# Performance work log

Measured on AMD Instinct MI355X. Metric: run time of the kernel, lower is better.

Reference implementation:

```python
import jax, jax.numpy as jnp
import numpy as np
from functools import partial

B, C, H, W = 16, 512, 38, 50
IMG_H, IMG_W = 608, 800
STRIDE = 16
IMG_SCALE = 1.0
MIN_SIZE = 16.0 * IMG_SCALE
PRE_NMS_TOP_N = 6000
POST_NMS_TOP_N = 300
NMS_THRESH = 0.7


def generate_anchor_base(base_size=16.0, ratios=(0.5, 1.0, 2.0), scales=(8.0, 16.0, 32.0)):
    # chainercv-style base anchors centered at (base/2, base/2), y1x1y2x2
    py = px = base_size / 2.0
    out = []
    for r in ratios:
        for s in scales:
            h = base_size * s * np.sqrt(r)
            w = base_size * s * np.sqrt(1.0 / r)
            out.append([py - h / 2, px - w / 2, py + h / 2, px + w / 2])
    return jnp.asarray(np.array(out, dtype=np.float32))  # [9, 4]


def all_anchors(anchor_base, stride, h, w):
    sy = jnp.arange(h, dtype=jnp.float32) * stride
    sx = jnp.arange(w, dtype=jnp.float32) * stride
    yy, xx = jnp.meshgrid(sy, sx, indexing='ij')
    shifts = jnp.stack([yy, xx, yy, xx], axis=-1).reshape(-1, 1, 4)  # [H*W,1,4]
    return (shifts + anchor_base[None]).reshape(-1, 4)  # [H*W*9, 4]


def conv2d(x, w, b, pad):
    y = jax.lax.conv_general_dilated(
        x, w, window_strides=(1, 1), padding=[(pad, pad), (pad, pad)],
        dimension_numbers=('NCHW', 'OIHW', 'NCHW'))
    return y + b[None, :, None, None]


def decode_boxes(anchors, loc):
    # anchors [N,4] y1x1y2x2, loc [B,N,4] (dy,dx,dh,dw)
    ah = anchors[:, 2] - anchors[:, 0]
    aw = anchors[:, 3] - anchors[:, 1]
    acy = anchors[:, 0] + 0.5 * ah
    acx = anchors[:, 1] + 0.5 * aw
    cy = loc[..., 0] * ah + acy
    cx = loc[..., 1] * aw + acx
    h = jnp.exp(loc[..., 2]) * ah
    w = jnp.exp(loc[..., 3]) * aw
    return jnp.stack([cy - 0.5 * h, cx - 0.5 * w, cy + 0.5 * h, cx + 0.5 * w], axis=-1)


def nms_fixed(boxes, scores, iou_thresh, max_out):
    # boxes [N,4], scores [N] (-inf = invalid); greedy NMS, fixed max_out steps
    areas = jnp.clip(boxes[:, 2] - boxes[:, 0], 0) * jnp.clip(boxes[:, 3] - boxes[:, 1], 0)

    def step(valid, _):
        s = jnp.where(valid, scores, -jnp.inf)
        i = jnp.argmax(s)
        ok = jnp.isfinite(s[i])
        box = boxes[i]
        yy1 = jnp.maximum(box[0], boxes[:, 0])
        xx1 = jnp.maximum(box[1], boxes[:, 1])
        yy2 = jnp.minimum(box[2], boxes[:, 2])
        xx2 = jnp.minimum(box[3], boxes[:, 3])
        inter = jnp.clip(yy2 - yy1, 0) * jnp.clip(xx2 - xx1, 0)
        iou = inter / (areas + areas[i] - inter + 1e-9)
        valid = valid & (iou <= iou_thresh)
        valid = valid.at[i].set(False)
        return valid, (i, ok)

    valid0 = jnp.isfinite(scores)
    _, (idx, ok) = jax.lax.scan(step, valid0, None, length=max_out)
    return idx, ok


def proposal_single(boxes, scores):
    # boxes [N,4], scores [N] for one image
    # clip to image
    boxes = jnp.stack([
        jnp.clip(boxes[:, 0], 0.0, IMG_H), jnp.clip(boxes[:, 1], 0.0, IMG_W),
        jnp.clip(boxes[:, 2], 0.0, IMG_H), jnp.clip(boxes[:, 3], 0.0, IMG_W)], axis=-1)
    hs = boxes[:, 2] - boxes[:, 0]
    ws = boxes[:, 3] - boxes[:, 1]
    keep = (hs >= MIN_SIZE) & (ws >= MIN_SIZE)
    scores = jnp.where(keep, scores, -jnp.inf)
    top_s, top_i = jax.lax.top_k(scores, PRE_NMS_TOP_N)
    top_b = boxes[top_i]
    idx, ok = nms_fixed(top_b, top_s, NMS_THRESH, POST_NMS_TOP_N)
    okf = ok.astype(boxes.dtype)
    rois = top_b[idx] * okf[:, None]
    rsc = jnp.where(ok, top_s[idx], 0.0)
    return jnp.concatenate([rois, rsc[:, None]], axis=-1)  # [POST, 5]


def setup_inputs() -> dict:
    key = jax.random.key(0)
    ks = jax.random.split(key, 7)
    return {
        'x': jax.random.normal(ks[0], (B, C, H, W), jnp.float32),
        'share_w': jax.random.normal(ks[1], (512, 512, 3, 3), jnp.float32) * 0.02,
        'share_b': jnp.zeros((512,), jnp.float32),
        'cls_w': jax.random.normal(ks[2], (18, 512, 1, 1), jnp.float32) * 0.02,
        'cls_b': jnp.zeros((18,), jnp.float32),
        'reg_w': jax.random.normal(ks[3], (36, 512, 1, 1), jnp.float32) * 0.02,
        'reg_b': jnp.zeros((36,), jnp.float32),
    }


def reference(x, share_w, share_b, cls_w, cls_b, reg_w, reg_b):
    anchors = all_anchors(generate_anchor_base(), STRIDE, H, W)  # [H*W*9, 4]
    shared = jax.nn.relu(conv2d(x, share_w, share_b, 1))
    cls = conv2d(shared, cls_w, cls_b, 0)           # [B,18,H,W]
    # note: original _reshape is a no-op (view result discarded), so softmax is over all 18 channels
    cls = jax.nn.softmax(cls, axis=1)
    reg = conv2d(shared, reg_w, reg_b, 0)           # [B,36,H,W]
    # foreground scores: [B,18,H,W] -> [B,H,W,9,2] -> fg channel
    scores = cls.transpose(0, 2, 3, 1).reshape(B, H * W * 9, 2)[..., 1]
    loc = reg.transpose(0, 2, 3, 1).reshape(B, H * W * 9, 4)
    boxes = decode_boxes(anchors, loc)              # [B,N,4]
    rois = jax.vmap(proposal_single)(boxes, scores)  # [B,POST,5]
    return rois
```

## Files before the change

kernel.cpp:

```cpp
#include <hip/hip_runtime.h>
#include <math.h>

#define NB 16
#define NC 512
#define NH 38
#define NW 50
#define NHW 1900
#define NPOS 30400
#define NANCH 17100
#define PRE_N 6000
#define POST_N 300
#define KTOT 4608
#define NIT 576
#define IMGH 608.0f
#define IMGW 800.0f

__global__ __launch_bounds__(256, 4)
void conv_f64_v7(const float* __restrict__ x, const float* __restrict__ w,
                 const float* __restrict__ bias, float* __restrict__ out)
{
    const int b    = blockIdx.z;
    const int co0  = blockIdx.y * 128;
    const int pos0 = blockIdx.x * 64;

    __shared__ __align__(16) double Ad[2][8][130];
    __shared__ __align__(16) double Bd[2][8][64];

    const int tid = threadIdx.x;
    const int ty  = tid >> 4;
    const int tx  = tid & 15;

    double acc[8][4];
#pragma unroll
    for (int m = 0; m < 8; ++m)
#pragma unroll
        for (int n = 0; n < 4; ++n) acc[m][n] = 0.0;

    const float* xb = x + (size_t)b * NC * NHW;

    const int coiA = tid >> 1;
    const int k4A  = (tid & 1) * 4;
    const float* wptr = w + (size_t)(co0 + coiA) * KTOT + k4A;

    const int kkB  = tid >> 5;
    const int piB  = tid & 31;
    const int pB1  = pos0 + piB;
    const int pB2  = pos0 + piB + 32;
    const int py1  = pB1 / NW, px1 = pB1 - (pB1 / NW) * NW;
    const int py2  = pB2 / NW, px2 = pB2 - (pB2 / NW) * NW;
    const bool ok1 = pB1 < NHW;
    const bool ok2 = pB2 < NHW;

    int ci = 0;
    int ky = kkB / 3;
    int kx = kkB - 3 * (kkB / 3);
    const float* xci = xb;

    float4 wa = *reinterpret_cast<const float4*>(wptr);
    float bs0, bs1;
    {
        const int yy1 = py1 + ky - 1, xx1 = px1 + kx - 1;
        const int yy2 = py2 + ky - 1, xx2 = px2 + kx - 1;
        bs0 = (ok1 && (unsigned)yy1 < (unsigned)NH && (unsigned)xx1 < (unsigned)NW)
                  ? xci[yy1 * NW + xx1] : 0.f;
        bs1 = (ok2 && (unsigned)yy2 < (unsigned)NH && (unsigned)xx2 < (unsigned)NW)
                  ? xci[yy2 * NW + xx2] : 0.f;
    }
    {
        const bool wrap = (ky == 0) && (kx == 0);
        if (wrap) { ky = 2; kx = 2; }
        else {
            --kx;
            if (kx < 0) { kx = 2; --ky; }
            ++ci; xci += NHW;
        }
    }
    Ad[0][k4A + 0][coiA] = (double)wa.x;
    Ad[0][k4A + 1][coiA] = (double)wa.y;
    Ad[0][k4A + 2][coiA] = (double)wa.z;
    Ad[0][k4A + 3][coiA] = (double)wa.w;
    Bd[0][kkB][piB]      = (double)bs0;
    Bd[0][kkB][piB + 32] = (double)bs1;
    __syncthreads();

    int cur = 0;
    for (int it = 0; it < NIT; ++it) {
        const bool more = (it + 1) < NIT;
        if (more) {
            wptr += 8;
            wa = *reinterpret_cast<const float4*>(wptr);
            const int yy1 = py1 + ky - 1, xx1 = px1 + kx - 1;
            const int yy2 = py2 + ky - 1, xx2 = px2 + kx - 1;
            bs0 = (ok1 && (unsigned)yy1 < (unsigned)NH && (unsigned)xx1 < (unsigned)NW)
                      ? xci[yy1 * NW + xx1] : 0.f;
            bs1 = (ok2 && (unsigned)yy2 < (unsigned)NH && (unsigned)xx2 < (unsigned)NW)
                      ? xci[yy2 * NW + xx2] : 0.f;
            const bool wrap = (ky == 0) && (kx == 0);
            if (wrap) { ky = 2; kx = 2; }
            else {
                --kx;
                if (kx < 0) { kx = 2; --ky; }
                ++ci; xci += NHW;
            }
        }

#pragma unroll
        for (int kk = 0; kk < 8; ++kk) {
            double av[8], bv[4];
#pragma unroll
            for (int m = 0; m < 8; ++m) av[m] = Ad[cur][kk][ty * 8 + m];
#pragma unroll
            for (int n = 0; n < 4; ++n) bv[n] = Bd[cur][kk][n * 16 + tx];
#pragma unroll
            for (int m = 0; m < 8; ++m)
#pragma unroll
                for (int n = 0; n < 4; ++n) acc[m][n] += av[m] * bv[n];
        }

        if (more) {
            const int nb = cur ^ 1;
            Ad[nb][k4A + 0][coiA] = (double)wa.x;
            Ad[nb][k4A + 1][coiA] = (double)wa.y;
            Ad[nb][k4A + 2][coiA] = (double)wa.z;
            Ad[nb][k4A + 3][coiA] = (double)wa.w;
            Bd[nb][kkB][piB]      = (double)bs0;
            Bd[nb][kkB][piB + 32] = (double)bs1;
            __syncthreads();
        }
        cur ^= 1;
    }

#pragma unroll
    for (int m = 0; m < 8; ++m) {
        const int co = co0 + ty * 8 + m;
        const double bi = (double)bias[co];
        float* orow = out + ((size_t)b * NC + co) * NHW;
#pragma unroll
        for (int n = 0; n < 4; ++n) {
            const int pos = pos0 + n * 16 + tx;
            if (pos < NHW) {
                const double d = acc[m][n] + bi;
                orow[pos] = (float)(d > 0.0 ? d : 0.0);
            }
        }
    }
}

__global__ __launch_bounds__(256)
void head_f64(const float* __restrict__ act,
              const float* __restrict__ cls_w, const float* __restrict__ cls_b,
              const float* __restrict__ reg_w, const float* __restrict__ reg_b,
              float* __restrict__ boxes, float* __restrict__ scores)
{
    const int p = blockIdx.x * 256 + threadIdx.x;
    if (p >= NPOS) return;
    const int b  = p / NHW;
    const int hw = p - b * NHW;

    const float* av = act + (size_t)b * NC * NHW + hw;

    double acc[54];
#pragma unroll
    for (int o = 0; o < 54; ++o) acc[o] = 0.0;

    for (int c = 0; c < NC; ++c) {
        const double v = (double)av[(size_t)c * NHW];
#pragma unroll
        for (int o = 0; o < 18; ++o) acc[o]      += v * (double)cls_w[o * NC + c];
#pragma unroll
        for (int o = 0; o < 36; ++o) acc[18 + o] += v * (double)reg_w[o * NC + c];
    }

    float lg[18];
#pragma unroll
    for (int o = 0; o < 18; ++o) lg[o] = (float)(acc[o] + (double)cls_b[o]);
    float loc[36];
#pragma unroll
    for (int o = 0; o < 36; ++o) loc[o] = (float)(acc[18 + o] + (double)reg_b[o]);

    double mx = -1e300;
#pragma unroll
    for (int o = 0; o < 18; ++o) mx = fmax(mx, (double)lg[o]);
    double sum = 0.0;
#pragma unroll
    for (int o = 0; o < 18; ++o) sum += exp((double)lg[o] - mx);
    const double inv = 1.0 / sum;

    const int hy = hw / NW;
    const int hx = hw - hy * NW;
    const float shy = (float)(hy * 16);
    const float shx = (float)(hx * 16);

    const double rats[3] = {0.5, 1.0, 2.0};
    const double scls[3] = {8.0, 16.0, 32.0};

#pragma unroll
    for (int a = 0; a < 9; ++a) {
        const int ir = a / 3, is = a - ir * 3;
        const double hh = 16.0 * scls[is] * sqrt(rats[ir]);
        const double wd = 16.0 * scls[is] * sqrt(1.0 / rats[ir]);
        const float ay1 = (float)(8.0 - hh * 0.5) + shy;
        const float ax1 = (float)(8.0 - wd * 0.5) + shx;
        const float ay2 = (float)(8.0 + hh * 0.5) + shy;
        const float ax2 = (float)(8.0 + wd * 0.5) + shx;
        const float ahf = ay2 - ay1;
        const float awf = ax2 - ax1;
        const float acy = ay1 + 0.5f * ahf;
        const float acx = ax1 + 0.5f * awf;

        const double ah = (double)ahf, aw = (double)awf;
        const double dy = (double)loc[4 * a + 0];
        const double dx = (double)loc[4 * a + 1];
        const double dh = (double)loc[4 * a + 2];
        const double dw = (double)loc[4 * a + 3];
        const double cy = dy * ah + (double)acy;
        const double cx = dx * aw + (double)acx;
        const double bh = exp(dh) * ah;
        const double bw = exp(dw) * aw;
        float y1 = (float)(cy - 0.5 * bh);
        float x1 = (float)(cx - 0.5 * bw);
        float y2 = (float)(cy + 0.5 * bh);
        float x2 = (float)(cx + 0.5 * bw);
        y1 = fminf(fmaxf(y1, 0.f), IMGH);
        y2 = fminf(fmaxf(y2, 0.f), IMGH);
        x1 = fminf(fmaxf(x1, 0.f), IMGW);
        x2 = fminf(fmaxf(x2, 0.f), IMGW);
        const bool keep = ((y2 - y1) >= 16.0f) && ((x2 - x1) >= 16.0f);

        float sc = (float)(exp((double)lg[2 * a + 1] - mx) * inv);
        if (!keep) sc = -INFINITY;

        const int n = hw * 9 + a;
        float4 bx; bx.x = y1; bx.y = x1; bx.z = y2; bx.w = x2;
        *reinterpret_cast<float4*>(&boxes[((size_t)b * NANCH + n) * 4]) = bx;
        scores[(size_t)b * NANCH + n] = sc;
    }
}

__global__ __launch_bounds__(256)
void rank2(const float* __restrict__ scores, const float* __restrict__ boxes,
           float* __restrict__ sortedS, float* __restrict__ sortedB)
{
    const int b = blockIdx.y;
    const int i = blockIdx.x * 256 + threadIdx.x;
    if (i >= NANCH) return;
    const float si = scores[(size_t)b * NANCH + i];
    const float* sb = scores + (size_t)b * NANCH;
    int rank = 0;
    for (int j = 0; j < NANCH; ++j) {
        const float sj = sb[j];
        rank += (sj > si) || (sj == si && j < i);
    }
    if (rank < PRE_N) {
        sortedS[(size_t)b * PRE_N + rank] = si;
        const float4 bx = *reinterpret_cast<const float4*>(&boxes[((size_t)b * NANCH + i) * 4]);
        *reinterpret_cast<float4*>(&sortedB[((size_t)b * PRE_N + rank) * 4]) = bx;
    }
}

__global__ __launch_bounds__(64)
void nms3(const float* __restrict__ sortedS, const float* __restrict__ sortedB,
          float* __restrict__ out)
{
    const int b    = blockIdx.x;
    const int lane = threadIdx.x;

    __shared__ float ky1[POST_N], kx1[POST_N], ky2[POST_N], kx2[POST_N];
    __shared__ float kar[POST_N], ksc[POST_N];
    __shared__ float cs[256];
    __shared__ float cb[256][4];

    const float* SS = sortedS + (size_t)b * PRE_N;
    const float* BB = sortedB + (size_t)b * PRE_N * 4;

    int nk = 0;
    bool done = false;
    for (int c0 = 0; c0 < PRE_N && !done; c0 += 256) {
        __syncthreads();
        for (int i = lane; i < 256; i += 64) {
            const int gi = c0 + i;
            if (gi < PRE_N) {
                cs[i] = SS[gi];
                const float4 bx = *reinterpret_cast<const float4*>(&BB[(size_t)gi * 4]);
                cb[i][0] = bx.x; cb[i][1] = bx.y; cb[i][2] = bx.z; cb[i][3] = bx.w;
            } else {
                cs[i] = -INFINITY;
                cb[i][0] = 0.f; cb[i][1] = 0.f; cb[i][2] = 0.f; cb[i][3] = 0.f;
            }
        }
        __syncthreads();

        for (int ic = 0; ic < 256; ++ic) {
            const float sc = cs[ic];
            if (sc == -INFINITY) { done = true; break; }
            const float y1 = cb[ic][0], x1 = cb[ic][1];
            const float y2 = cb[ic][2], x2 = cb[ic][3];
            const float areaC = fmaxf(y2 - y1, 0.f) * fmaxf(x2 - x1, 0.f);
            bool sup = false;
            for (int t = lane; t < nk; t += 64) {
                const float yy1 = fmaxf(y1, ky1[t]);
                const float xx1 = fmaxf(x1, kx1[t]);
                const float yy2 = fminf(y2, ky2[t]);
                const float xx2 = fminf(x2, kx2[t]);
                const float inter = fmaxf(yy2 - yy1, 0.f) * fmaxf(xx2 - xx1, 0.f);
                const float iou = inter / (areaC + kar[t] - inter + 1e-9f);
                if (iou > 0.7f) sup = true;
            }
            if (__ballot(sup) == 0ull) {
                if (lane == 0) {
                    ky1[nk] = y1; kx1[nk] = x1; ky2[nk] = y2; kx2[nk] = x2;
                    kar[nk] = areaC; ksc[nk] = sc;
                }
                __syncthreads();
                ++nk;
                if (nk == POST_N) { done = true; break; }
            }
        }
    }

    __syncthreads();
    for (int k2 = lane; k2 < POST_N; k2 += 64) {
        float o0 = 0.f, o1 = 0.f, o2 = 0.f, o3 = 0.f, o4 = 0.f;
        if (k2 < nk) {
            o0 = ky1[k2]; o1 = kx1[k2]; o2 = ky2[k2]; o3 = kx2[k2]; o4 = ksc[k2];
        }
        float* orow = out + ((size_t)b * POST_N + k2) * 5;
        orow[0] = o0; orow[1] = o1; orow[2] = o2; orow[3] = o3; orow[4] = o4;
    }
}

static const float* pick_input(void* const* d_in, const int* in_sizes, int n_in,
                               int want, int fallback)
{
    for (int i = 0; i < n_in; ++i)
        if (in_sizes[i] == want) return (const float*)d_in[i];
    return (const float*)d_in[fallback];
}

extern "C" void kernel_launch(void* const* d_in, const int* in_sizes, int n_in,
                              void* d_out, int out_size, void* d_ws, size_t ws_size,
                              hipStream_t stream)
{
    const float* x       = pick_input(d_in, in_sizes, n_in, 15564800, 0);
    const float* share_w = pick_input(d_in, in_sizes, n_in, 2359296, 1);
    const float* share_b = pick_input(d_in, in_sizes, n_in, 512, 2);
    const float* cls_w   = pick_input(d_in, in_sizes, n_in, 9216, 3);
    const float* cls_b   = pick_input(d_in, in_sizes, n_in, 18, 4);
    const float* reg_w   = pick_input(d_in, in_sizes, n_in, 18432, 5);
    const float* reg_b   = pick_input(d_in, in_sizes, n_in, 36, 6);
    float* out = (float*)d_out;

    float* W = (float*)d_ws;
    float* act     = W;
    float* boxes   = W + 15564800;
    float* scores  = W + 16659200;
    float* sortedB = W + 16932800;
    float* sortedS = W + 17316800;

    conv_f64_v7<<<dim3(30, 4, NB), 256, 0, stream>>>(x, share_w, share_b, act);

    head_f64<<<dim3(119), 256, 0, stream>>>(act, cls_w, cls_b, reg_w, reg_b,
                                            boxes, scores);

    rank2<<<dim3(67, 16), 256, 0, stream>>>(scores, boxes, sortedS, sortedB);

    nms3<<<dim3(16), 64, 0, stream>>>(sortedS, sortedB, out);
}
```

Baseline: 4.999 ms.

## Split 1x1 head convolution across output-channel groups into separate kernel

The 1x1 cls/reg head, which ran as 119 blocks each holding 54 double accumulators per thread, is split into a head_part kernel over a 119x6 grid that computes 9 output channels per thread and writes logits to a workspace buffer. A new decode_k kernel then reads those logits to do the softmax and box decoding. This is meant to raise parallelism and cut register pressure on an undersubscribed GPU. In exchange it adds an extra launch, a workspace round-trip for the logits, and reads the activations six times instead of once.

```diff
diff --git a/kernel.cpp b/kernel.cpp
--- a/kernel.cpp
+++ b/kernel.cpp
@@ -147,9 +147,46 @@
 }
 
 __global__ __launch_bounds__(256)
-void head_f64(const float* __restrict__ act,
-              const float* __restrict__ cls_w, const float* __restrict__ cls_b,
-              const float* __restrict__ reg_w, const float* __restrict__ reg_b,
+void head_part(const float* __restrict__ act,
+               const float* __restrict__ cls_w, const float* __restrict__ cls_b,
+               const float* __restrict__ reg_w, const float* __restrict__ reg_b,
+               float* __restrict__ hl)
+{
+    const int p = blockIdx.x * 256 + threadIdx.x;
+    if (p >= NPOS) return;
+    const int g  = blockIdx.y;
+    const int b  = p / NHW;
+    const int hw = p - b * NHW;
+
+    const float* av = act + (size_t)b * NC * NHW + hw;
+
+    const float* wrow[9];
+    double bia[9];
+#pragma unroll
+    for (int j = 0; j < 9; ++j) {
+        const int o = g * 9 + j;
+        if (o < 18) { wrow[j] = cls_w + (size_t)o * NC;        bia[j] = (double)cls_b[o]; }
+        else        { wrow[j] = reg_w + (size_t)(o - 18) * NC; bia[j] = (double)reg_b[o - 18]; }
+    }
+
+    double acc[9];
+#pragma unroll
+    for (int j = 0; j < 9; ++j) acc[j] = 0.0;
+
+    for (int c = 0; c < NC; ++c) {
+        const double v = (double)av[(size_t)c * NHW];
+#pragma unroll
+        for (int j = 0; j < 9; ++j) acc[j] += v * (double)wrow[j][c];
+    }
+
+    float* hb = hl + (size_t)b * 54 * NHW + hw;
+#pragma unroll
+    for (int j = 0; j < 9; ++j)
+        hb[(size_t)(g * 9 + j) * NHW] = (float)(acc[j] + bia[j]);
+}
+
+__global__ __launch_bounds__(256)
+void decode_k(const float* __restrict__ hl,
               float* __restrict__ boxes, float* __restrict__ scores)
 {
     const int p = blockIdx.x * 256 + threadIdx.x;
@@ -157,26 +194,14 @@
     const int b  = p / NHW;
     const int hw = p - b * NHW;
 
-    const float* av = act + (size_t)b * NC * NHW + hw;
-
-    double acc[54];
-#pragma unroll
-    for (int o = 0; o < 54; ++o) acc[o] = 0.0;
-
-    for (int c = 0; c < NC; ++c) {
-        const double v = (double)av[(size_t)c * NHW];
-#pragma unroll
-        for (int o = 0; o < 18; ++o) acc[o]      += v * (double)cls_w[o * NC + c];
-#pragma unroll
-        for (int o = 0; o < 36; ++o) acc[18 + o] += v * (double)reg_w[o * NC + c];
-    }
+    const float* hb = hl + (size_t)b * 54 * NHW + hw;
 
     float lg[18];
 #pragma unroll
-    for (int o = 0; o < 18; ++o) lg[o] = (float)(acc[o] + (double)cls_b[o]);
+    for (int o = 0; o < 18; ++o) lg[o] = hb[(size_t)o * NHW];
     float loc[36];
 #pragma unroll
-    for (int o = 0; o < 36; ++o) loc[o] = (float)(acc[18 + o] + (double)reg_b[o]);
+    for (int o = 0; o < 36; ++o) loc[o] = hb[(size_t)(18 + o) * NHW];
 
     double mx = -1e300;
 #pragma unroll
@@ -356,11 +381,14 @@
     float* scores  = W + 16659200;
     float* sortedB = W + 16932800;
     float* sortedS = W + 17316800;
+    float* hl      = W + 17412800;
 
     conv_f64_v7<<<dim3(30, 4, NB), 256, 0, stream>>>(x, share_w, share_b, act);
 
-    head_f64<<<dim3(119), 256, 0, stream>>>(act, cls_w, cls_b, reg_w, reg_b,
-                                            boxes, scores);
+    head_part<<<dim3(119, 6), 256, 0, stream>>>(act, cls_w, cls_b,
+                                                reg_w, reg_b, hl);
+
+    decode_k<<<dim3(119), 256, 0, stream>>>(hl, boxes, scores);
 
     rank2<<<dim3(67, 16), 256, 0, stream>>>(scores, boxes, sortedS, sortedB);
 
```

New measurement: 4.999 ms. About the same (-0.0%).
